# Optimization experiments

Measured on AMD Instinct MI355X. Metric: run time of the kernel, lower is better.

The kernel has to match this reference:

```python
import jax, jax.numpy as jnp
import numpy as np

_EPS = 1e-4  # pytorch3d se3_exp_map clamps the SQUARED rotation angle at this eps


def _hat(w):
    # w: [..., 3] -> skew-symmetric [..., 3, 3]
    wx, wy, wz = w[..., 0], w[..., 1], w[..., 2]
    z = jnp.zeros_like(wx)
    return jnp.stack([
        jnp.stack([z, -wz, wy], axis=-1),
        jnp.stack([wz, z, -wx], axis=-1),
        jnp.stack([-wy, wx, z], axis=-1),
    ], axis=-2)


def _se3_exp(dofs):
    # dofs: [..., 6] = (log_translation, log_rotation), pytorch3d convention.
    # Returns R [..., 3, 3] and t [..., 3] such that p' = R @ p + t,
    # matching pytorch3d's row-convention matrix M ([:3,:3]=R^T, [3,:3]=t)
    # applied as p' = p @ M[:3,:3] + M[3,:3].
    t_log = dofs[..., :3]
    w = dofs[..., 3:]
    nrms = jnp.sum(w * w, axis=-1)
    theta = jnp.sqrt(jnp.clip(nrms, _EPS))  # [...]
    H = _hat(w)
    H2 = H @ H
    st, ct = jnp.sin(theta), jnp.cos(theta)
    f1 = (st / theta)[..., None, None]
    f2 = ((1.0 - ct) / (theta * theta))[..., None, None]
    f3 = ((theta - st) / (theta * theta * theta))[..., None, None]
    I = jnp.eye(3, dtype=dofs.dtype)
    R = I + f1 * H + f2 * H2            # Rodrigues
    V = I + f2 * H + f3 * H2            # left-Jacobian of SO(3)
    t = jnp.einsum('...ij,...j->...i', V, t_log)
    return R, t


def setup_inputs() -> dict:
    key = jax.random.key(0)
    k1, k2 = jax.random.split(key)
    B, T, N = 64, 28, 4096
    X_v = jax.random.normal(k1, (B, T, N, 3), dtype=jnp.float32)
    dofs = jax.random.normal(k2, (B, T, 6), dtype=jnp.float32)
    return {"X_v": X_v, "dofs": dofs}


def reference(X_v, dofs):
    # Fused, fully-batched version of the per-tooth python loop:
    # one SE3 exp over all (B,T) transforms + one batched point transform.
    R, t = _se3_exp(dofs)                                  # [B,T,3,3], [B,T,3]
    out = jnp.einsum('btij,btnj->btni', R, X_v) + t[:, :, None, :]
    return out
```

## Files before the change

kernel.cpp:

```cpp
#include <hip/hip_runtime.h>


typedef float f4 __attribute__((ext_vector_type(4)));

__global__ __launch_bounds__(256) void se3_pre(
    const float* __restrict__ dofs, float* __restrict__ ws, int BT)
{
    const int i = blockIdx.x * 256 + threadIdx.x;
    if (i >= BT) return;
    const float* d = dofs + i * 6;
    const float tx = d[0], ty = d[1], tz = d[2];
    const float wx = d[3], wy = d[4], wz = d[5];

    const float nrm2  = wx * wx + wy * wy + wz * wz;
    const float th2   = fmaxf(nrm2, 1e-4f);
    const float theta = sqrtf(th2);
    const float st = sinf(theta);
    const float ct = cosf(theta);
    const float f1 = st / theta;
    const float f2 = (1.0f - ct) / th2;
    const float f3 = (theta - st) / (th2 * theta);

    const float xx = wx * wx, yy = wy * wy, zz = wz * wz;
    const float xy = wx * wy, xz = wx * wz, yz = wy * wz;

    const float R00 = 1.0f - f2 * (yy + zz);
    const float R01 = f2 * xy - f1 * wz;
    const float R02 = f2 * xz + f1 * wy;
    const float R10 = f2 * xy + f1 * wz;
    const float R11 = 1.0f - f2 * (xx + zz);
    const float R12 = f2 * yz - f1 * wx;
    const float R20 = f2 * xz - f1 * wy;
    const float R21 = f2 * yz + f1 * wx;
    const float R22 = 1.0f - f2 * (xx + yy);

    const float V00 = 1.0f - f3 * (yy + zz);
    const float V01 = f3 * xy - f2 * wz;
    const float V02 = f3 * xz + f2 * wy;
    const float V10 = f3 * xy + f2 * wz;
    const float V11 = 1.0f - f3 * (xx + zz);
    const float V12 = f3 * yz - f2 * wx;
    const float V20 = f3 * xz - f2 * wy;
    const float V21 = f3 * yz + f2 * wx;
    const float V22 = 1.0f - f3 * (xx + yy);

    const float Tx = V00 * tx + V01 * ty + V02 * tz;
    const float Ty = V10 * tx + V11 * ty + V12 * tz;
    const float Tz = V20 * tx + V21 * ty + V22 * tz;

    f4* W = (f4*)(ws + (long long)i * 16);
    W[0] = (f4){R00, R01, R02, Tx};
    W[1] = (f4){R10, R11, R12, Ty};
    W[2] = (f4){R20, R21, R22, Tz};
}

__global__ __launch_bounds__(256) void se3_stream(
    const float* __restrict__ X, const float* __restrict__ ws,
    float* __restrict__ out, int n3, int tilesPerBT)
{
    const int bt   = blockIdx.x / tilesPerBT;
    const int tile = blockIdx.x - bt * tilesPerBT;
    const int t    = threadIdx.x;

    const int fInBT = tile * 6144 + t * 24;
    const long long baseF = (long long)bt * (long long)n3 + (long long)fInBT;
    const f4* __restrict__ Xp = (const f4*)(X + baseF);
    f4* __restrict__ Op       = (f4*)(out + baseF);

    const bool full = (fInBT + 24) <= n3;
    f4 v0, v1, v2, v3, v4, v5;
    if (full) {
        v0 = Xp[0]; v1 = Xp[1]; v2 = Xp[2];
        v3 = Xp[3]; v4 = Xp[4]; v5 = Xp[5];
    }

    const f4* __restrict__ W = (const f4*)(ws + (long long)bt * 16);
    const f4 w0 = W[0], w1 = W[1], w2 = W[2];

    if (full) {
        const float s[24] = {v0.x, v0.y, v0.z, v0.w, v1.x, v1.y, v1.z, v1.w,
                             v2.x, v2.y, v2.z, v2.w, v3.x, v3.y, v3.z, v3.w,
                             v4.x, v4.y, v4.z, v4.w, v5.x, v5.y, v5.z, v5.w};
        float r[24];
#pragma unroll
        for (int k = 0; k < 8; ++k) {
            const float x = s[3 * k], y = s[3 * k + 1], z = s[3 * k + 2];
            r[3 * k]     = fmaf(w0.x, x, fmaf(w0.y, y, fmaf(w0.z, z, w0.w)));
            r[3 * k + 1] = fmaf(w1.x, x, fmaf(w1.y, y, fmaf(w1.z, z, w1.w)));
            r[3 * k + 2] = fmaf(w2.x, x, fmaf(w2.y, y, fmaf(w2.z, z, w2.w)));
        }
        Op[0] = (f4){r[0],  r[1],  r[2],  r[3]};
        Op[1] = (f4){r[4],  r[5],  r[6],  r[7]};
        Op[2] = (f4){r[8],  r[9],  r[10], r[11]};
        Op[3] = (f4){r[12], r[13], r[14], r[15]};
        Op[4] = (f4){r[16], r[17], r[18], r[19]};
        Op[5] = (f4){r[20], r[21], r[22], r[23]};
    } else {
        const long long base = (long long)bt * (long long)n3;
        for (int f = fInBT; f + 3 <= n3 && f < fInBT + 24; f += 3) {
            const float px = X[base + f + 0], py = X[base + f + 1], pz = X[base + f + 2];
            out[base + f + 0] = fmaf(w0.x, px, fmaf(w0.y, py, fmaf(w0.z, pz, w0.w)));
            out[base + f + 1] = fmaf(w1.x, px, fmaf(w1.y, py, fmaf(w1.z, pz, w1.w)));
            out[base + f + 2] = fmaf(w2.x, px, fmaf(w2.y, py, fmaf(w2.z, pz, w2.w)));
        }
    }
}

__device__ __forceinline__ float rfl(float x) {
    return __uint_as_float(__builtin_amdgcn_readfirstlane(__float_as_uint(x)));
}

__global__ __launch_bounds__(256) void se3_apply_fused(
    const float* __restrict__ X, const float* __restrict__ dofs,
    float* __restrict__ out, int n3, int tilesPerBT)
{
    const int bt   = blockIdx.x / tilesPerBT;
    const int tile = blockIdx.x - bt * tilesPerBT;
    const int t    = threadIdx.x;
    const int fInBT = tile * 3072 + t * 12;
    const long long baseF = (long long)bt * (long long)n3 + (long long)fInBT;
    const f4* __restrict__ Xp = (const f4*)(X + baseF);
    f4* __restrict__ Op       = (f4*)(out + baseF);

    const bool full = (fInBT + 12) <= n3;
    f4 v0, v1, v2;
    if (full) { v0 = Xp[0]; v1 = Xp[1]; v2 = Xp[2]; }

    const float* d = dofs + bt * 6;
    const float tx = d[0], ty = d[1], tz = d[2];
    const float wx = d[3], wy = d[4], wz = d[5];
    const float nrm2  = wx * wx + wy * wy + wz * wz;
    const float th2   = fmaxf(nrm2, 1e-4f);
    const float theta = sqrtf(th2);
    const float st = sinf(theta), ct = cosf(theta);
    const float f1 = st / theta;
    const float f2 = (1.0f - ct) / th2;
    const float f3 = (theta - st) / (th2 * theta);
    const float xx = wx * wx, yy = wy * wy, zz = wz * wz;
    const float xy = wx * wy, xz = wx * wz, yz = wy * wz;
    const float R00 = rfl(1.0f - f2 * (yy + zz));
    const float R01 = rfl(f2 * xy - f1 * wz);
    const float R02 = rfl(f2 * xz + f1 * wy);
    const float R10 = rfl(f2 * xy + f1 * wz);
    const float R11 = rfl(1.0f - f2 * (xx + zz));
    const float R12 = rfl(f2 * yz - f1 * wx);
    const float R20 = rfl(f2 * xz - f1 * wy);
    const float R21 = rfl(f2 * yz + f1 * wx);
    const float R22 = rfl(1.0f - f2 * (xx + yy));
    const float V00 = 1.0f - f3 * (yy + zz);
    const float V01 = f3 * xy - f2 * wz;
    const float V02 = f3 * xz + f2 * wy;
    const float V10 = f3 * xy + f2 * wz;
    const float V11 = 1.0f - f3 * (xx + zz);
    const float V12 = f3 * yz - f2 * wx;
    const float V20 = f3 * xz - f2 * wy;
    const float V21 = f3 * yz + f2 * wx;
    const float V22 = 1.0f - f3 * (xx + yy);
    const float Tx = rfl(V00 * tx + V01 * ty + V02 * tz);
    const float Ty = rfl(V10 * tx + V11 * ty + V12 * tz);
    const float Tz = rfl(V20 * tx + V21 * ty + V22 * tz);

    if (full) {
        const float x0 = v0.x, y0 = v0.y, z0 = v0.z;
        const float x1 = v0.w, y1 = v1.x, z1 = v1.y;
        const float x2 = v1.z, y2 = v1.w, z2 = v2.x;
        const float x3 = v2.y, y3 = v2.z, z3 = v2.w;
        f4 o0, o1, o2;
        o0.x = fmaf(R00, x0, fmaf(R01, y0, fmaf(R02, z0, Tx)));
        o0.y = fmaf(R10, x0, fmaf(R11, y0, fmaf(R12, z0, Ty)));
        o0.z = fmaf(R20, x0, fmaf(R21, y0, fmaf(R22, z0, Tz)));
        o0.w = fmaf(R00, x1, fmaf(R01, y1, fmaf(R02, z1, Tx)));
        o1.x = fmaf(R10, x1, fmaf(R11, y1, fmaf(R12, z1, Ty)));
        o1.y = fmaf(R20, x1, fmaf(R21, y1, fmaf(R22, z1, Tz)));
        o1.z = fmaf(R00, x2, fmaf(R01, y2, fmaf(R02, z2, Tx)));
        o1.w = fmaf(R10, x2, fmaf(R11, y2, fmaf(R12, z2, Ty)));
        o2.x = fmaf(R20, x2, fmaf(R21, y2, fmaf(R22, z2, Tz)));
        o2.y = fmaf(R00, x3, fmaf(R01, y3, fmaf(R02, z3, Tx)));
        o2.z = fmaf(R10, x3, fmaf(R11, y3, fmaf(R12, z3, Ty)));
        o2.w = fmaf(R20, x3, fmaf(R21, y3, fmaf(R22, z3, Tz)));
        Op[0] = o0; Op[1] = o1; Op[2] = o2;
    } else {
        const long long base = (long long)bt * (long long)n3;
        for (int f = fInBT; f + 3 <= n3 && f < fInBT + 12; f += 3) {
            const float px = X[base + f + 0], py = X[base + f + 1], pz = X[base + f + 2];
            out[base + f + 0] = fmaf(R00, px, fmaf(R01, py, fmaf(R02, pz, Tx)));
            out[base + f + 1] = fmaf(R10, px, fmaf(R11, py, fmaf(R12, pz, Ty)));
            out[base + f + 2] = fmaf(R20, px, fmaf(R21, py, fmaf(R22, pz, Tz)));
        }
    }
}

extern "C" void kernel_launch(void* const* d_in, const int* in_sizes, int n_in,
                              void* d_out, int out_size, void* d_ws, size_t ws_size,
                              hipStream_t stream) {
    const float* X    = (const float*)d_in[0];
    const float* dofs = (const float*)d_in[1];
    float* out        = (float*)d_out;

    const int BT = in_sizes[1] / 6;
    const int n3 = in_sizes[0] / BT;

    const size_t wsNeed = (size_t)BT * 16 * sizeof(float);
    if (d_ws != nullptr && ws_size >= wsNeed) {
        float* ws = (float*)d_ws;
        const int preBlocks = (BT + 255) / 256;
        se3_pre<<<dim3((unsigned)preBlocks), 256, 0, stream>>>(dofs, ws, BT);

        const int tilesPerBT = (n3 + 6143) / 6144;
        dim3 grid((unsigned)(BT * tilesPerBT));
        se3_stream<<<grid, 256, 0, stream>>>(X, ws, out, n3, tilesPerBT);
    } else {
        const int tilesPerBT = (n3 + 3071) / 3072;
        dim3 grid((unsigned)(BT * tilesPerBT));
        se3_apply_fused<<<grid, 256, 0, stream>>>(X, dofs, out, n3, tilesPerBT);
    }
}
```

Measured before the change: 167.0 us.

## Replace streaming kernel with persistent per-BT software-pipelined loop

The streaming kernel, which ran one block per 6144-float tile, is replaced by one block per (b,t) pair. Each block loops over its points with inline-asm global_load_dwordx4 prefetches into a double buffer and manual s_waitcnt control, so loads for the next iterations overlap with compute and stores. This cuts the block count and the per-block setup cost. The grid drops to BT=1792 blocks, which may reduce occupancy and the memory-level parallelism across the GPU. The path is only taken when n3 is a multiple of 3072.

```diff
diff --git a/kernel.cpp b/kernel.cpp
--- a/kernel.cpp
+++ b/kernel.cpp
@@ -54,54 +54,82 @@
     W[2] = (f4){R20, R21, R22, Tz};
 }
 
-__global__ __launch_bounds__(256) void se3_stream(
+
+#define PREF(b0, b1, b2, sIdx)                                                 \
+    do {                                                                       \
+        const f4* _p = (const f4*)(Xbt + (sIdx) * 12);                         \
+        asm volatile("global_load_dwordx4 %0, %3, off\n\t"                     \
+                     "global_load_dwordx4 %1, %3, off offset:16\n\t"           \
+                     "global_load_dwordx4 %2, %3, off offset:32"               \
+                     : "=&v"(b0), "=&v"(b1), "=&v"(b2)                         \
+                     : "v"(_p)                                                 \
+                     : "memory");                                              \
+    } while (0)
+
+#define CSTORE(b0, b1, b2, sIdx)                                               \
+    do {                                                                       \
+        const float x0 = b0.x, y0 = b0.y, z0 = b0.z;                           \
+        const float x1 = b0.w, y1 = b1.x, z1 = b1.y;                           \
+        const float x2 = b1.z, y2 = b1.w, z2 = b2.x;                           \
+        const float x3 = b2.y, y3 = b2.z, z3 = b2.w;                           \
+        f4 o0, o1, o2;                                                         \
+        o0.x = fmaf(w0.x, x0, fmaf(w0.y, y0, fmaf(w0.z, z0, w0.w)));           \
+        o0.y = fmaf(w1.x, x0, fmaf(w1.y, y0, fmaf(w1.z, z0, w1.w)));           \
+        o0.z = fmaf(w2.x, x0, fmaf(w2.y, y0, fmaf(w2.z, z0, w2.w)));           \
+        o0.w = fmaf(w0.x, x1, fmaf(w0.y, y1, fmaf(w0.z, z1, w0.w)));           \
+        o1.x = fmaf(w1.x, x1, fmaf(w1.y, y1, fmaf(w1.z, z1, w1.w)));           \
+        o1.y = fmaf(w2.x, x1, fmaf(w2.y, y1, fmaf(w2.z, z1, w2.w)));           \
+        o1.z = fmaf(w0.x, x2, fmaf(w0.y, y2, fmaf(w0.z, z2, w0.w)));           \
+        o1.w = fmaf(w1.x, x2, fmaf(w1.y, y2, fmaf(w1.z, z2, w1.w)));           \
+        o2.x = fmaf(w2.x, x2, fmaf(w2.y, y2, fmaf(w2.z, z2, w2.w)));           \
+        o2.y = fmaf(w0.x, x3, fmaf(w0.y, y3, fmaf(w0.z, z3, w0.w)));           \
+        o2.z = fmaf(w1.x, x3, fmaf(w1.y, y3, fmaf(w1.z, z3, w1.w)));           \
+        o2.w = fmaf(w2.x, x3, fmaf(w2.y, y3, fmaf(w2.z, z3, w2.w)));           \
+        f4* _op = (f4*)(Obt + (sIdx) * 12);                                    \
+        _op[0] = o0; _op[1] = o1; _op[2] = o2;                                 \
+    } while (0)
+
+__device__ __forceinline__ void waitv(int c) {
+    if (c >= 6)      { asm volatile("s_waitcnt vmcnt(6)" ::: "memory"); }
+    else if (c == 3) { asm volatile("s_waitcnt vmcnt(3)" ::: "memory"); }
+    else             { asm volatile("s_waitcnt vmcnt(0)" ::: "memory"); }
+    __builtin_amdgcn_sched_barrier(0);
+}
+
+__global__ __launch_bounds__(256) void se3_pipe(
     const float* __restrict__ X, const float* __restrict__ ws,
-    float* __restrict__ out, int n3, int tilesPerBT)
+    float* __restrict__ out, int n3, int slotsPerBT)
 {
-    const int bt   = blockIdx.x / tilesPerBT;
-    const int tile = blockIdx.x - bt * tilesPerBT;
-    const int t    = threadIdx.x;
-
-    const int fInBT = tile * 6144 + t * 24;
-    const long long baseF = (long long)bt * (long long)n3 + (long long)fInBT;
-    const f4* __restrict__ Xp = (const f4*)(X + baseF);
-    f4* __restrict__ Op       = (f4*)(out + baseF);
-
-    const bool full = (fInBT + 24) <= n3;
-    f4 v0, v1, v2, v3, v4, v5;
-    if (full) {
-        v0 = Xp[0]; v1 = Xp[1]; v2 = Xp[2];
-        v3 = Xp[3]; v4 = Xp[4]; v5 = Xp[5];
-    }
-
-    const f4* __restrict__ W = (const f4*)(ws + (long long)bt * 16);
-    const f4 w0 = W[0], w1 = W[1], w2 = W[2];
-
-    if (full) {
-        const float s[24] = {v0.x, v0.y, v0.z, v0.w, v1.x, v1.y, v1.z, v1.w,
-                             v2.x, v2.y, v2.z, v2.w, v3.x, v3.y, v3.z, v3.w,
-                             v4.x, v4.y, v4.z, v4.w, v5.x, v5.y, v5.z, v5.w};
-        float r[24];
-#pragma unroll
-        for (int k = 0; k < 8; ++k) {
-            const float x = s[3 * k], y = s[3 * k + 1], z = s[3 * k + 2];
-            r[3 * k]     = fmaf(w0.x, x, fmaf(w0.y, y, fmaf(w0.z, z, w0.w)));
-            r[3 * k + 1] = fmaf(w1.x, x, fmaf(w1.y, y, fmaf(w1.z, z, w1.w)));
-            r[3 * k + 2] = fmaf(w2.x, x, fmaf(w2.y, y, fmaf(w2.z, z, w2.w)));
+    const int bt = blockIdx.x;
+    const int t  = threadIdx.x;
+    const float* __restrict__ Xbt = X   + (long long)bt * n3;
+    float*       __restrict__ Obt = out + (long long)bt * n3;
+
+    const f4* Wp = (const f4*)(ws + (long long)bt * 16);
+    const f4 w0 = Wp[0], w1 = Wp[1], w2 = Wp[2];
+    asm volatile("" :: "v"(w0), "v"(w1), "v"(w2));
+    asm volatile("s_waitcnt vmcnt(0) lgkmcnt(0)" ::: "memory");
+    __builtin_amdgcn_sched_barrier(0);
+
+    const int nIter = slotsPerBT >> 8;
+
+    f4 A0, A1, A2, B0, B1, B2;
+    PREF(A0, A1, A2, t);
+    if (nIter > 1) PREF(B0, B1, B2, t + 256);
+
+    int i = 0;
+    while (i < nIter) {
+        {
+            waitv(3 * (i >= 1) + 3 * ((i + 1) < nIter));
+            CSTORE(A0, A1, A2, t + 256 * i);
+            if (i + 2 < nIter) PREF(A0, A1, A2, t + 256 * (i + 2));
+            ++i;
         }
-        Op[0] = (f4){r[0],  r[1],  r[2],  r[3]};
-        Op[1] = (f4){r[4],  r[5],  r[6],  r[7]};
-        Op[2] = (f4){r[8],  r[9],  r[10], r[11]};
-        Op[3] = (f4){r[12], r[13], r[14], r[15]};
-        Op[4] = (f4){r[16], r[17], r[18], r[19]};
-        Op[5] = (f4){r[20], r[21], r[22], r[23]};
-    } else {
-        const long long base = (long long)bt * (long long)n3;
-        for (int f = fInBT; f + 3 <= n3 && f < fInBT + 24; f += 3) {
-            const float px = X[base + f + 0], py = X[base + f + 1], pz = X[base + f + 2];
-            out[base + f + 0] = fmaf(w0.x, px, fmaf(w0.y, py, fmaf(w0.z, pz, w0.w)));
-            out[base + f + 1] = fmaf(w1.x, px, fmaf(w1.y, py, fmaf(w1.z, pz, w1.w)));
-            out[base + f + 2] = fmaf(w2.x, px, fmaf(w2.y, py, fmaf(w2.z, pz, w2.w)));
+        if (i < nIter) {
+            waitv(3 + 3 * ((i + 1) < nIter));
+            CSTORE(B0, B1, B2, t + 256 * i);
+            if (i + 2 < nIter) PREF(B0, B1, B2, t + 256 * (i + 2));
+            ++i;
         }
     }
 }
@@ -201,14 +229,13 @@
     const int n3 = in_sizes[0] / BT;
 
     const size_t wsNeed = (size_t)BT * 16 * sizeof(float);
-    if (d_ws != nullptr && ws_size >= wsNeed) {
+    if (d_ws != nullptr && ws_size >= wsNeed && (n3 % 3072) == 0) {
         float* ws = (float*)d_ws;
         const int preBlocks = (BT + 255) / 256;
         se3_pre<<<dim3((unsigned)preBlocks), 256, 0, stream>>>(dofs, ws, BT);
 
-        const int tilesPerBT = (n3 + 6143) / 6144;
-        dim3 grid((unsigned)(BT * tilesPerBT));
-        se3_stream<<<grid, 256, 0, stream>>>(X, ws, out, n3, tilesPerBT);
+        const int slotsPerBT = n3 / 12;
+        se3_pipe<<<dim3((unsigned)BT), 256, 0, stream>>>(X, ws, out, n3, slotsPerBT);
     } else {
         const int tilesPerBT = (n3 + 3071) / 3072;
         dim3 grid((unsigned)(BT * tilesPerBT));
```

After: 163.2 us. 1.02x faster.
